# Performance work log

Measured on AMD Instinct MI355X. Metric: run time of the kernel, lower is better.

The kernel has to match this reference:

```python
import jax, jax.numpy as jnp
import numpy as np

B, I, H = 4096, 2048, 2048


def setup_inputs() -> dict:
    key = jax.random.key(0)
    k1, k2, k3, k4, k5 = jax.random.split(key, 5)
    return {
        "x": jax.random.normal(k1, (B, I), dtype=jnp.float32),
        "coefficients": jax.random.normal(k2, (I, H), dtype=jnp.float32) * 0.1,
        "amplitude_an": jax.random.normal(k3, (1, I, H), dtype=jnp.float32) * 0.1,
        "amplitude_bn": jax.random.normal(k4, (1, I, H), dtype=jnp.float32) * 0.1,
        "bias": jax.random.normal(k5, (1, I), dtype=jnp.float32),
    }


def reference(x, coefficients, amplitude_an, amplitude_bn, bias):
    # phase[b,h] = x[b,:] @ coefficients[:,h]  (same matmul done per-sample in torch loop)
    phase = x @ coefficients  # [B, H]
    num_harmonics = coefficients.shape[1]
    # sum over harmonics of an[i,h]*cos(phase[b,h]) + bn[i,h]*sin(phase[b,h])
    gain = (
        jnp.einsum("bh,ih->bi", jnp.cos(phase), amplitude_an[0])
        + jnp.einsum("bh,ih->bi", jnp.sin(phase), amplitude_bn[0])
        + num_harmonics * bias  # bias added per-harmonic before the sum over H
    )
    return gain  # [B, I]
```

## Files before the change

### kernel.cpp

```cpp
#include <hip/hip_runtime.h>
#include <hip/hip_bf16.h>

#define B_DIM 4096
#define I_DIM 2048
#define H_DIM 2048

typedef unsigned char u8;
typedef unsigned short u16;
typedef unsigned int u32;
typedef __attribute__((ext_vector_type(4))) float f32x4;
typedef __attribute__((ext_vector_type(4))) int i32x4;
typedef __attribute__((ext_vector_type(8))) int i32x8;

__device__ __forceinline__ void gload_lds16(const void* g, void* l) {
  __builtin_amdgcn_global_load_lds(
      (const __attribute__((address_space(1))) void*)g,
      (__attribute__((address_space(3))) void*)l, 16, 0, 0);
}

__device__ __forceinline__ u32 f2fp4(float v, float inv_scale) {
  const float a = fabsf(v) * inv_scale;
  u32 m = (u32)(a > 0.25f) + (u32)(a > 0.75f) + (u32)(a > 1.25f) +
          (u32)(a > 1.75f) + (u32)(a > 2.5f) + (u32)(a > 3.5f) + (u32)(a > 5.0f);
  return ((__float_as_uint(v) >> 31) << 3) | m;
}

__global__ void convert_ew(const float* __restrict__ x, const float* __restrict__ an,
                           const float* __restrict__ bn, u16* __restrict__ xf4,
                           u32* __restrict__ ab4) {
  const long NX4 = (long)B_DIM * I_DIM / 4;
  const long NA4 = (long)I_DIM * H_DIM / 4;
  const long total = NX4 + NA4;
  for (long t = (long)blockIdx.x * blockDim.x + threadIdx.x; t < total;
       t += (long)gridDim.x * blockDim.x) {
    if (t < NX4) {
      float4 v = *(const float4*)(x + t * 4);
      u32 b0 = f2fp4(v.x, 1.f) | (f2fp4(v.y, 1.f) << 4);
      u32 b1 = f2fp4(v.z, 1.f) | (f2fp4(v.w, 1.f) << 4);
      xf4[t] = (u16)(b0 | (b1 << 8));
    } else {
      long p = (t - NX4) * 4;
      float4 va = *(const float4*)(an + p);
      float4 vb = *(const float4*)(bn + p);
      u32 b0 = f2fp4(va.x, 8.f) | (f2fp4(vb.x, 8.f) << 4);
      u32 b1 = f2fp4(va.y, 8.f) | (f2fp4(vb.y, 8.f) << 4);
      u32 b2 = f2fp4(va.z, 8.f) | (f2fp4(vb.z, 8.f) << 4);
      u32 b3 = f2fp4(va.w, 8.f) | (f2fp4(vb.w, 8.f) << 4);
      ab4[p >> 2] = b0 | (b1 << 8) | (b2 << 16) | (b3 << 24);
    }
  }
}

__global__ void transpose_conv(const float* __restrict__ c, u16* __restrict__ ct4) {
  __shared__ float tile[32][33];
  const int i0 = blockIdx.y * 32;
  const int h0 = blockIdx.x * 32;
  const int tid = threadIdx.x;
  const int tx = tid & 31;
  const int ty = tid >> 5;
  for (int r = ty; r < 32; r += 8)
    tile[r][tx] = c[(long)(i0 + r) * H_DIM + (h0 + tx)];
  __syncthreads();
  const int hl = tid >> 3;
  const int q = (tid & 7) * 4;
  u32 w = f2fp4(tile[q + 0][hl], 8.f) | (f2fp4(tile[q + 1][hl], 8.f) << 4) |
          (f2fp4(tile[q + 2][hl], 8.f) << 8) | (f2fp4(tile[q + 3][hl], 8.f) << 12);
  ct4[(long)(h0 + hl) * (I_DIM / 4) + ((i0 + q) >> 2)] = (u16)w;
}

#define NBUF 49152

__device__ __forceinline__ void stage_tile(const char* Ab, const char* Bb, long kbyte,
                                           long lda, long ldb, char* buf, int tid) {
#pragma unroll
  for (int i = 0; i < 2; ++i) {
    const int o = i * 8192 + tid * 16;
    const int row = o >> 7;
    const int ls = ((((o >> 4) & 7) ^ (row & 7)) << 4);
    gload_lds16(Ab + (long)row * lda + kbyte + ls, buf + o);
  }
#pragma unroll
  for (int i = 0; i < 4; ++i) {
    const int o = i * 8192 + tid * 16;
    const int row = o >> 7;
    const int ls = ((((o >> 4) & 7) ^ (row & 7)) << 4);
    gload_lds16(Bb + (long)row * ldb + kbyte + ls, buf + 16384 + o);
  }
}

__device__ __forceinline__ i32x4 frag_ld16(const char* S, int row, int slot) {
  return *(const i32x4*)(S + row * 128 + ((slot ^ (row & 7)) << 4));
}

template <int SA, int SB>
__device__ __forceinline__ void gemm_kloop_fp4(const char* __restrict__ A,
                                               const char* __restrict__ Bt,
                                               int rowA0, int colB0, long Kbytes,
                                               char* smem, f32x4 acc[4][4]) {
  const int tid = threadIdx.x;
  const int lane = tid & 63;
  const int wid = tid >> 6;
  const int wr = wid >> 2;
  const int wc = wid & 3;
  const long lda = Kbytes, ldb = Kbytes;
  const char* Ab = A + (long)rowA0 * lda;
  const char* Bb = Bt + (long)colB0 * ldb;
  const int arow = wr * 64 + (lane & 15);
  const int brow = wc * 64 + (lane & 15);
  const int g = lane >> 4;
  const int nt = (int)(Kbytes >> 7);

  char* b0 = smem;
  char* b1 = smem + NBUF;
  char* b2 = smem + 2 * NBUF;

  stage_tile(Ab, Bb, 0, lda, ldb, b0, tid);
  stage_tile(Ab, Bb, 128, lda, ldb, b1, tid);

  for (int t = 0; t < nt; ++t) {
    if (t < nt - 1) asm volatile("s_waitcnt vmcnt(6)" ::: "memory");
    else            asm volatile("s_waitcnt vmcnt(0)" ::: "memory");
    __builtin_amdgcn_sched_barrier(0);
    __builtin_amdgcn_s_barrier();
    __builtin_amdgcn_sched_barrier(0);

    i32x8 af[8], bfr[8];
#pragma unroll
    for (int s = 0; s < 2; ++s)
#pragma unroll
      for (int m = 0; m < 4; ++m)
        *(i32x4*)&af[s * 4 + m] = frag_ld16(b0, arow + m * 16, s * 4 + g);
#pragma unroll
    for (int s = 0; s < 2; ++s)
#pragma unroll
      for (int n = 0; n < 4; ++n)
        *(i32x4*)&bfr[s * 4 + n] = frag_ld16(b0 + 16384, brow + n * 16, s * 4 + g);

    if (t + 2 < nt)
      stage_tile(Ab, Bb, (long)(t + 2) * 128, lda, ldb, b2, tid);
    __builtin_amdgcn_sched_barrier(0);
    asm volatile("s_waitcnt lgkmcnt(0)" ::: "memory");
    __builtin_amdgcn_sched_barrier(0);

    __builtin_amdgcn_s_setprio(1);
#pragma unroll
    for (int s = 0; s < 2; ++s)
#pragma unroll
      for (int m = 0; m < 4; ++m)
#pragma unroll
        for (int n = 0; n < 4; ++n)
          acc[m][n] = __builtin_amdgcn_mfma_scale_f32_16x16x128_f8f6f4(
              af[s * 4 + m], bfr[s * 4 + n], acc[m][n], 4, 4, 0, SA, 0, SB);
    __builtin_amdgcn_s_setprio(0);
    __builtin_amdgcn_sched_barrier(0);

    char* tmp = b0; b0 = b1; b1 = b2; b2 = tmp;
  }
}

__device__ __forceinline__ void tile_xy(int& bx, int& by) {
  const int bid = blockIdx.x;
  const int id = (bid & 7) * 32 + (bid >> 3);
  bx = id & 7;
  by = id >> 3;
}

__global__ __launch_bounds__(512, 1) void gemm_phase(const char* __restrict__ xf4,
                                                     const char* __restrict__ ct4,
                                                     u8* __restrict__ cs4) {
  __shared__ __align__(16) char smem[3 * NBUF];
  int bx, by;
  tile_xy(bx, by);
  const int rowA0 = by * 128;
  const int colB0 = bx * 256;
  f32x4 acc[4][4];
#pragma unroll
  for (int m = 0; m < 4; ++m)
#pragma unroll
    for (int n = 0; n < 4; ++n)
#pragma unroll
      for (int j = 0; j < 4; ++j) acc[m][n][j] = 0.0f;

  gemm_kloop_fp4<0x7F7F7F7F, 0x7C7C7C7C>(xf4, ct4, rowA0, colB0, I_DIM / 2, smem, acc);

  const int lane = threadIdx.x & 63;
  const int wid = threadIdx.x >> 6;
  const int wr = wid >> 2, wc = wid & 3;
#pragma unroll
  for (int m = 0; m < 4; ++m) {
#pragma unroll
    for (int n = 0; n < 4; ++n) {
      const int col = colB0 + wc * 64 + n * 16 + (lane & 15);
#pragma unroll
      for (int j = 0; j < 4; ++j) {
        const int row = rowA0 + wr * 64 + m * 16 + (lane >> 4) * 4 + j;
        const float p = acc[m][n][j];
        const u32 b = f2fp4(__cosf(p), 4.f) | (f2fp4(__sinf(p), 4.f) << 4);
        cs4[(long)row * H_DIM + col] = (u8)b;
      }
    }
  }
}

__global__ __launch_bounds__(512, 1) void gemm_gain(const char* __restrict__ cs4,
                                                    const char* __restrict__ ab4,
                                                    const float* __restrict__ bias,
                                                    float* __restrict__ out) {
  __shared__ __align__(16) char smem[3 * NBUF];
  int bx, by;
  tile_xy(bx, by);
  const int rowA0 = by * 128;
  const int colB0 = bx * 256;
  f32x4 acc[4][4];
#pragma unroll
  for (int m = 0; m < 4; ++m)
#pragma unroll
    for (int n = 0; n < 4; ++n)
#pragma unroll
      for (int j = 0; j < 4; ++j) acc[m][n][j] = 0.0f;

  gemm_kloop_fp4<0x7D7D7D7D, 0x7C7C7C7C>(cs4, ab4, rowA0, colB0, H_DIM, smem, acc);

  const int lane = threadIdx.x & 63;
  const int wid = threadIdx.x >> 6;
  const int wr = wid >> 2, wc = wid & 3;
#pragma unroll
  for (int m = 0; m < 4; ++m) {
#pragma unroll
    for (int n = 0; n < 4; ++n) {
      const int col = colB0 + wc * 64 + n * 16 + (lane & 15);
      const float bv = 2048.0f * bias[col];
#pragma unroll
      for (int j = 0; j < 4; ++j) {
        const int row = rowA0 + wr * 64 + m * 16 + (lane >> 4) * 4 + j;
        out[(long)row * I_DIM + col] = acc[m][n][j] + bv;
      }
    }
  }
}

extern "C" void kernel_launch(void* const* d_in, const int* in_sizes, int n_in,
                              void* d_out, int out_size, void* d_ws, size_t ws_size,
                              hipStream_t stream) {
  const float* x     = (const float*)d_in[0];
  const float* coeff = (const float*)d_in[1];
  const float* an    = (const float*)d_in[2];
  const float* bn    = (const float*)d_in[3];
  const float* bias  = (const float*)d_in[4];
  float* out = (float*)d_out;

  char* ws = (char*)d_ws;
  char* xf4 = ws;
  char* ct4 = ws + (4L << 20);
  char* ab4 = ws + (8L << 20);
  u8*  cs4  = (u8*)(ws + (12L << 20));

  convert_ew<<<1024, 256, 0, stream>>>(x, an, bn, (u16*)xf4, (u32*)ab4);
  transpose_conv<<<dim3(H_DIM / 32, I_DIM / 32), 256, 0, stream>>>(coeff, (u16*)ct4);
  gemm_phase<<<256, 512, 0, stream>>>(xf4, ct4, cs4);
  gemm_gain<<<256, 512, 0, stream>>>((const char*)cs4, (const char*)ab4, bias, out);
}
```

Baseline: 67.05 us.

## Fuse prep kernels, interleave staging with MFMA sub-steps, regroup tile-to-XCD mapping

Merges the elementwise FP4 conversion and the coefficient transpose-conversion into one launch, which removes a kernel launch and lets the two pieces of work overlap. The GEMM k-loop is split into four quarter-steps, each issuing part of the next tile's global-to-LDS loads between MFMA groups, so load issue is spread across the compute. This adds extra workgroup barriers per iteration. The tile-to-block mapping also changes so that each XCD gets a compact 4x8 region of tiles, aiming at better L2 reuse.

```diff
diff --git a/kernel.cpp b/kernel.cpp
--- a/kernel.cpp
+++ b/kernel.cpp
@@ -12,6 +12,8 @@
 typedef __attribute__((ext_vector_type(4))) int i32x4;
 typedef __attribute__((ext_vector_type(8))) int i32x8;
 
+#define SBAR __builtin_amdgcn_sched_barrier(0)
+
 __device__ __forceinline__ void gload_lds16(const void* g, void* l) {
   __builtin_amdgcn_global_load_lds(
       (const __attribute__((address_space(1))) void*)g,
@@ -25,14 +27,33 @@
   return ((__float_as_uint(v) >> 31) << 3) | m;
 }
 
-__global__ void convert_ew(const float* __restrict__ x, const float* __restrict__ an,
-                           const float* __restrict__ bn, u16* __restrict__ xf4,
-                           u32* __restrict__ ab4) {
+__global__ void prep_all(const float* __restrict__ x, const float* __restrict__ coeff,
+                         const float* __restrict__ an, const float* __restrict__ bn,
+                         u16* __restrict__ xf4, u16* __restrict__ ct4,
+                         u32* __restrict__ ab4) {
+  if (blockIdx.x < 4096) {
+    __shared__ float tile[32][33];
+    const int h0 = (blockIdx.x & 63) * 32;
+    const int i0 = (blockIdx.x >> 6) * 32;
+    const int tid = threadIdx.x;
+    const int tx = tid & 31;
+    const int ty = tid >> 5;
+    for (int r = ty; r < 32; r += 8)
+      tile[r][tx] = coeff[(long)(i0 + r) * H_DIM + (h0 + tx)];
+    __syncthreads();
+    const int hl = tid >> 3;
+    const int q = (tid & 7) * 4;
+    u32 w = f2fp4(tile[q + 0][hl], 8.f) | (f2fp4(tile[q + 1][hl], 8.f) << 4) |
+            (f2fp4(tile[q + 2][hl], 8.f) << 8) | (f2fp4(tile[q + 3][hl], 8.f) << 12);
+    ct4[(long)(h0 + hl) * (I_DIM / 4) + ((i0 + q) >> 2)] = (u16)w;
+    return;
+  }
   const long NX4 = (long)B_DIM * I_DIM / 4;
   const long NA4 = (long)I_DIM * H_DIM / 4;
   const long total = NX4 + NA4;
-  for (long t = (long)blockIdx.x * blockDim.x + threadIdx.x; t < total;
-       t += (long)gridDim.x * blockDim.x) {
+  const long stride = (long)1024 * blockDim.x;
+  for (long t = (long)(blockIdx.x - 4096) * blockDim.x + threadIdx.x; t < total;
+       t += stride) {
     if (t < NX4) {
       float4 v = *(const float4*)(x + t * 4);
       u32 b0 = f2fp4(v.x, 1.f) | (f2fp4(v.y, 1.f) << 4);
@@ -51,41 +72,21 @@
   }
 }
 
-__global__ void transpose_conv(const float* __restrict__ c, u16* __restrict__ ct4) {
-  __shared__ float tile[32][33];
-  const int i0 = blockIdx.y * 32;
-  const int h0 = blockIdx.x * 32;
-  const int tid = threadIdx.x;
-  const int tx = tid & 31;
-  const int ty = tid >> 5;
-  for (int r = ty; r < 32; r += 8)
-    tile[r][tx] = c[(long)(i0 + r) * H_DIM + (h0 + tx)];
-  __syncthreads();
-  const int hl = tid >> 3;
-  const int q = (tid & 7) * 4;
-  u32 w = f2fp4(tile[q + 0][hl], 8.f) | (f2fp4(tile[q + 1][hl], 8.f) << 4) |
-          (f2fp4(tile[q + 2][hl], 8.f) << 8) | (f2fp4(tile[q + 3][hl], 8.f) << 12);
-  ct4[(long)(h0 + hl) * (I_DIM / 4) + ((i0 + q) >> 2)] = (u16)w;
-}
-
 #define NBUF 49152
 
-__device__ __forceinline__ void stage_tile(const char* Ab, const char* Bb, long kbyte,
-                                           long lda, long ldb, char* buf, int tid) {
-#pragma unroll
-  for (int i = 0; i < 2; ++i) {
-    const int o = i * 8192 + tid * 16;
-    const int row = o >> 7;
-    const int ls = ((((o >> 4) & 7) ^ (row & 7)) << 4);
-    gload_lds16(Ab + (long)row * lda + kbyte + ls, buf + o);
-  }
-#pragma unroll
-  for (int i = 0; i < 4; ++i) {
-    const int o = i * 8192 + tid * 16;
-    const int row = o >> 7;
-    const int ls = ((((o >> 4) & 7) ^ (row & 7)) << 4);
-    gload_lds16(Bb + (long)row * ldb + kbyte + ls, buf + 16384 + o);
-  }
+__device__ __forceinline__ void stageA1(const char* Ab, long kbyte, long lda,
+                                        char* buf, int tid, int i) {
+  const int o = i * 8192 + tid * 16;
+  const int row = o >> 7;
+  const int ls = ((((o >> 4) & 7) ^ (row & 7)) << 4);
+  gload_lds16(Ab + (long)row * lda + kbyte + ls, buf + o);
+}
+__device__ __forceinline__ void stageB1(const char* Bb, long kbyte, long ldb,
+                                        char* buf, int tid, int i) {
+  const int o = i * 8192 + tid * 16;
+  const int row = o >> 7;
+  const int ls = ((((o >> 4) & 7) ^ (row & 7)) << 4);
+  gload_lds16(Bb + (long)row * ldb + kbyte + ls, buf + 16384 + o);
 }
 
 __device__ __forceinline__ i32x4 frag_ld16(const char* S, int row, int slot) {
@@ -114,45 +115,98 @@
   char* b1 = smem + NBUF;
   char* b2 = smem + 2 * NBUF;
 
-  stage_tile(Ab, Bb, 0, lda, ldb, b0, tid);
-  stage_tile(Ab, Bb, 128, lda, ldb, b1, tid);
+#pragma unroll
+  for (int i = 0; i < 2; ++i) stageA1(Ab, 0, lda, b0, tid, i);
+#pragma unroll
+  for (int i = 0; i < 4; ++i) stageB1(Bb, 0, ldb, b0, tid, i);
+#pragma unroll
+  for (int i = 0; i < 2; ++i) stageA1(Ab, 128, lda, b1, tid, i);
+#pragma unroll
+  for (int i = 0; i < 4; ++i) stageB1(Bb, 128, ldb, b1, tid, i);
 
   for (int t = 0; t < nt; ++t) {
     if (t < nt - 1) asm volatile("s_waitcnt vmcnt(6)" ::: "memory");
     else            asm volatile("s_waitcnt vmcnt(0)" ::: "memory");
-    __builtin_amdgcn_sched_barrier(0);
+    SBAR;
     __builtin_amdgcn_s_barrier();
-    __builtin_amdgcn_sched_barrier(0);
-
-    i32x8 af[8], bfr[8];
-#pragma unroll
-    for (int s = 0; s < 2; ++s)
-#pragma unroll
-      for (int m = 0; m < 4; ++m)
-        *(i32x4*)&af[s * 4 + m] = frag_ld16(b0, arow + m * 16, s * 4 + g);
-#pragma unroll
-    for (int s = 0; s < 2; ++s)
-#pragma unroll
-      for (int n = 0; n < 4; ++n)
-        *(i32x4*)&bfr[s * 4 + n] = frag_ld16(b0 + 16384, brow + n * 16, s * 4 + g);
-
-    if (t + 2 < nt)
-      stage_tile(Ab, Bb, (long)(t + 2) * 128, lda, ldb, b2, tid);
-    __builtin_amdgcn_sched_barrier(0);
+    SBAR;
+
+    const bool st = (t + 2 < nt);
+    const long kb2 = (long)(t + 2) * 128;
+    i32x8 af[2][4], bfr[2][4];
+
+#pragma unroll
+    for (int m = 0; m < 4; ++m)
+      *(i32x4*)&af[0][m] = frag_ld16(b0, arow + m * 16, g);
+    *(i32x4*)&bfr[0][0] = frag_ld16(b0 + 16384, brow, g);
+    *(i32x4*)&bfr[0][1] = frag_ld16(b0 + 16384, brow + 16, g);
+    if (st) { stageA1(Ab, kb2, lda, b2, tid, 0); stageA1(Ab, kb2, lda, b2, tid, 1); }
+    SBAR;
     asm volatile("s_waitcnt lgkmcnt(0)" ::: "memory");
-    __builtin_amdgcn_sched_barrier(0);
-
+    SBAR;
     __builtin_amdgcn_s_setprio(1);
 #pragma unroll
-    for (int s = 0; s < 2; ++s)
-#pragma unroll
-      for (int m = 0; m < 4; ++m)
-#pragma unroll
-        for (int n = 0; n < 4; ++n)
-          acc[m][n] = __builtin_amdgcn_mfma_scale_f32_16x16x128_f8f6f4(
-              af[s * 4 + m], bfr[s * 4 + n], acc[m][n], 4, 4, 0, SA, 0, SB);
+    for (int m = 0; m < 4; ++m)
+#pragma unroll
+      for (int n = 0; n < 2; ++n)
+        acc[m][n] = __builtin_amdgcn_mfma_scale_f32_16x16x128_f8f6f4(
+            af[0][m], bfr[0][n], acc[m][n], 4, 4, 0, SA, 0, SB);
     __builtin_amdgcn_s_setprio(0);
-    __builtin_amdgcn_sched_barrier(0);
+    SBAR;
+    __builtin_amdgcn_s_barrier();
+
+#pragma unroll
+    for (int m = 0; m < 4; ++m)
+      *(i32x4*)&af[1][m] = frag_ld16(b0, arow + m * 16, 4 + g);
+    *(i32x4*)&bfr[0][2] = frag_ld16(b0 + 16384, brow + 32, g);
+    *(i32x4*)&bfr[0][3] = frag_ld16(b0 + 16384, brow + 48, g);
+    if (st) { stageB1(Bb, kb2, ldb, b2, tid, 0); stageB1(Bb, kb2, ldb, b2, tid, 1); }
+    SBAR;
+    asm volatile("s_waitcnt lgkmcnt(0)" ::: "memory");
+    SBAR;
+    __builtin_amdgcn_s_setprio(1);
+#pragma unroll
+    for (int m = 0; m < 4; ++m)
+#pragma unroll
+      for (int n = 2; n < 4; ++n)
+        acc[m][n] = __builtin_amdgcn_mfma_scale_f32_16x16x128_f8f6f4(
+            af[0][m], bfr[0][n], acc[m][n], 4, 4, 0, SA, 0, SB);
+    __builtin_amdgcn_s_setprio(0);
+    SBAR;
+    __builtin_amdgcn_s_barrier();
+
+    *(i32x4*)&bfr[1][0] = frag_ld16(b0 + 16384, brow, 4 + g);
+    *(i32x4*)&bfr[1][1] = frag_ld16(b0 + 16384, brow + 16, 4 + g);
+    if (st) stageB1(Bb, kb2, ldb, b2, tid, 2);
+    SBAR;
+    asm volatile("s_waitcnt lgkmcnt(0)" ::: "memory");
+    SBAR;
+    __builtin_amdgcn_s_setprio(1);
+#pragma unroll
+    for (int m = 0; m < 4; ++m)
+#pragma unroll
+      for (int n = 0; n < 2; ++n)
+        acc[m][n] = __builtin_amdgcn_mfma_scale_f32_16x16x128_f8f6f4(
+            af[1][m], bfr[1][n], acc[m][n], 4, 4, 0, SA, 0, SB);
+    __builtin_amdgcn_s_setprio(0);
+    SBAR;
+    __builtin_amdgcn_s_barrier();
+
+    *(i32x4*)&bfr[1][2] = frag_ld16(b0 + 16384, brow + 32, 4 + g);
+    *(i32x4*)&bfr[1][3] = frag_ld16(b0 + 16384, brow + 48, 4 + g);
+    if (st) stageB1(Bb, kb2, ldb, b2, tid, 3);
+    SBAR;
+    asm volatile("s_waitcnt lgkmcnt(0)" ::: "memory");
+    SBAR;
+    __builtin_amdgcn_s_setprio(1);
+#pragma unroll
+    for (int m = 0; m < 4; ++m)
+#pragma unroll
+      for (int n = 2; n < 4; ++n)
+        acc[m][n] = __builtin_amdgcn_mfma_scale_f32_16x16x128_f8f6f4(
+            af[1][m], bfr[1][n], acc[m][n], 4, 4, 0, SA, 0, SB);
+    __builtin_amdgcn_s_setprio(0);
+    SBAR;
 
     char* tmp = b0; b0 = b1; b1 = b2; b2 = tmp;
   }
@@ -160,9 +214,10 @@
 
 __device__ __forceinline__ void tile_xy(int& bx, int& by) {
   const int bid = blockIdx.x;
-  const int id = (bid & 7) * 32 + (bid >> 3);
-  bx = id & 7;
-  by = id >> 3;
+  const int xcd = bid & 7;
+  const int loc = bid >> 3;
+  bx = (xcd & 1) * 4 + (loc & 3);
+  by = (xcd >> 1) * 8 + (loc >> 2);
 }
 
 __global__ __launch_bounds__(512, 1) void gemm_phase(const char* __restrict__ xf4,
@@ -255,8 +310,8 @@
   char* ab4 = ws + (8L << 20);
   u8*  cs4  = (u8*)(ws + (12L << 20));
 
-  convert_ew<<<1024, 256, 0, stream>>>(x, an, bn, (u16*)xf4, (u32*)ab4);
-  transpose_conv<<<dim3(H_DIM / 32, I_DIM / 32), 256, 0, stream>>>(coeff, (u16*)ct4);
+  prep_all<<<5120, 256, 0, stream>>>(x, coeff, an, bn, (u16*)xf4, (u16*)ct4,
+                                     (u32*)ab4);
   gemm_phase<<<256, 512, 0, stream>>>(xf4, ct4, cs4);
   gemm_gain<<<256, 512, 0, stream>>>((const char*)cs4, (const char*)ab4, bias, out);
 }
```

Measured after the change: 67.69 us. No clear change (+1.0%).
